# Kernel tuning notes

Measured on AMD Instinct MI355X. Metric: run time of the kernel, lower is better.

Reference implementation:

```python
import jax, jax.numpy as jnp
import numpy as np

# OGB feature vocab sizes
ATOM_DIMS = [119, 4, 12, 12, 10, 6, 6, 2, 2]
BOND_DIMS = [5, 6, 2]
ATOM_OFF = np.concatenate([[0], np.cumsum(ATOM_DIMS)[:-1]]).astype(np.int32)
BOND_OFF = np.concatenate([[0], np.cumsum(BOND_DIMS)[:-1]]).astype(np.int32)
SCHEDULE_LEN = 5   # len(train_schedule) == len(eval_schedule)
NUM_GRAPHS = 12000
BN_EPS = 1e-5

N_NODES, N_EDGES, HIDDEN, NUM_TASKS = 300000, 600000, 128, 128


def setup_inputs() -> dict:
    key = jax.random.key(0)
    ks = jax.random.split(key, 16)
    x = jax.random.randint(ks[0], (N_NODES, 9), 0, 2, dtype=jnp.int32)
    edge_index = jax.random.randint(ks[1], (2, N_EDGES), 0, N_NODES, dtype=jnp.int32)
    edge_attr = jax.random.randint(ks[2], (N_EDGES, 3), 0, 2, dtype=jnp.int32)
    batch = jnp.sort(jax.random.randint(ks[3], (N_NODES,), 0, NUM_GRAPHS, dtype=jnp.int32))
    # learned parameters (embedding tables concatenated with offsets)
    atom_emb = jax.random.normal(ks[4], (sum(ATOM_DIMS), HIDDEN), jnp.float32) * 0.1
    bond_emb = jax.random.normal(ks[5], (sum(BOND_DIMS), HIDDEN), jnp.float32) * 0.1
    conv_W = jax.random.normal(ks[6], (HIDDEN, HIDDEN), jnp.float32) * (1.0 / np.sqrt(HIDDEN))
    conv_b = jnp.zeros((HIDDEN,), jnp.float32)
    root_emb = jax.random.normal(ks[7], (HIDDEN,), jnp.float32) * 0.1
    bn_gamma = jnp.ones((HIDDEN,), jnp.float32)
    bn_beta = jnp.zeros((HIDDEN,), jnp.float32)
    bn_mean = jnp.zeros((HIDDEN,), jnp.float32)   # running stats (eval mode)
    bn_var = jnp.ones((HIDDEN,), jnp.float32)
    lin_W = jax.random.normal(ks[8], (NUM_TASKS, HIDDEN), jnp.float32) * (1.0 / np.sqrt(HIDDEN))
    lin_b = jnp.zeros((NUM_TASKS,), jnp.float32)
    return {"x": x, "edge_index": edge_index, "edge_attr": edge_attr, "batch": batch,
            "atom_emb": atom_emb, "bond_emb": bond_emb, "conv_W": conv_W, "conv_b": conv_b,
            "root_emb": root_emb, "bn_gamma": bn_gamma, "bn_beta": bn_beta,
            "bn_mean": bn_mean, "bn_var": bn_var, "lin_W": lin_W, "lin_b": lin_b}


def reference(x, edge_index, edge_attr, batch, atom_emb, bond_emb, conv_W, conv_b,
              root_emb, bn_gamma, bn_beta, bn_mean, bn_var, lin_W, lin_b):
    N = x.shape[0]
    # AtomEncoder / BondEncoder: sum of per-feature embedding lookups
    h = atom_emb[x + jnp.asarray(ATOM_OFF, x.dtype)].sum(axis=1)            # [N, H]
    e = bond_emb[edge_attr + jnp.asarray(BOND_OFF, edge_attr.dtype)].sum(axis=1)  # [E, H]
    row, col = edge_index[0], edge_index[1]
    deg = jax.ops.segment_sum(jnp.ones_like(row, h.dtype), row, num_segments=N) + 1.0  # [N]
    dis = deg ** -0.5                                                        # deg >= 1, no inf
    norm = dis[row] * dis[col]                                               # [E]
    inv_std = bn_gamma / jnp.sqrt(bn_var + BN_EPS)
    for i in range(SCHEDULE_LEN):
        old = h
        z = h @ conv_W.T + conv_b                                            # [N, H]
        # message: norm * relu(x_j + edge_emb), aggregated at target (col) via scatter-add
        msg = norm[:, None] * jax.nn.relu(z[row] + e)                        # [E, H]
        agg = jax.ops.segment_sum(msg, col, num_segments=N)                  # [N, H]
        z = agg + jax.nn.relu(z + root_emb) / deg[:, None]                   # self-loop term
        z = jax.nn.relu(z)
        z = (z - bn_mean) * inv_std + bn_beta                                # BN (eval, running stats)
        # dropout: identity in eval mode
        # NOTE: faithful to source bug: smooth_fac is the loop index i, not schedule[i]
        h = i * old + (1 - i) * z
    # global mean pool over graphs
    counts = jax.ops.segment_sum(jnp.ones((N,), h.dtype), batch, num_segments=NUM_GRAPHS)
    pooled = jax.ops.segment_sum(h, batch, num_segments=NUM_GRAPHS) / jnp.maximum(counts, 1.0)[:, None]
    return pooled @ lin_W.T + lin_b                                          # [num_graphs, num_tasks]
```

## Files before the change

### kernel.cpp

```cpp
#include <hip/hip_runtime.h>

#define HID 128
#define AROWS 173

typedef __attribute__((ext_vector_type(8))) short short8;
typedef __attribute__((ext_vector_type(8))) unsigned short ushort8v;
typedef __attribute__((ext_vector_type(4))) float floatx4;
typedef __attribute__((ext_vector_type(4))) unsigned short ushort4v;

__device__ __forceinline__ unsigned short f2bf(float f) {
    unsigned u = __builtin_bit_cast(unsigned, f);
    u += 0x7FFF + ((u >> 16) & 1);
    return (unsigned short)(u >> 16);
}
__device__ __forceinline__ float bf2f(unsigned short s) {
    unsigned u = ((unsigned)s) << 16;
    return __builtin_bit_cast(float, u);
}

__global__ void fillrd_kernel(float* __restrict__ dis, int* __restrict__ indeg,
                              int* __restrict__ dhist, int N)
{
    int i = blockIdx.x * 256 + threadIdx.x;
    if (i < N) { dis[i] = 0.f; indeg[i] = 0; }
    if (blockIdx.x == 0 && threadIdx.x < 32) dhist[threadIdx.x] = 0;
}

__global__ void diag_kernel(float* __restrict__ out, long n, float val)
{
    long i = (long)blockIdx.x * blockDim.x + threadIdx.x;
    if (i < n) out[i] = val;
}

__global__ __launch_bounds__(256) void tables_kernel(
    const float* __restrict__ conv_W, unsigned short* __restrict__ Wb,
    const float* __restrict__ lin_W, unsigned short* __restrict__ linWb,
    const float* __restrict__ bond_emb, unsigned short* __restrict__ comb,
    const float* __restrict__ gamma, const float* __restrict__ beta,
    const float* __restrict__ mean, const float* __restrict__ var,
    float* __restrict__ bnsc, float* __restrict__ bnsh,
    const float* __restrict__ atom_emb, unsigned short* __restrict__ aeb)
{
    int blk = blockIdx.x;
    int tid = threadIdx.x;
    if (blk < 64) {
        int i = blk * 256 + tid;
        Wb[i] = f2bf(conv_W[i]);
    } else if (blk < 128) {
        int i = (blk - 64) * 256 + tid;
        linWb[i] = f2bf(lin_W[i]);
    } else if (blk < 158) {
        int i = (blk - 128) * 2 + (tid >> 7);
        int c = tid & 127;
        int a0 = i / 12, a1 = (i % 12) / 2, a2 = i % 2;
        comb[i * HID + c] = f2bf(bond_emb[a0 * HID + c] + bond_emb[(5 + a1) * HID + c]
                               + bond_emb[(11 + a2) * HID + c]);
    } else if (blk == 158) {
        if (tid < HID) {
            float sc = gamma[tid] * rsqrtf(var[tid] + 1e-5f);
            bnsc[tid] = sc;
            bnsh[tid] = beta[tid] - mean[tid] * sc;
        }
    } else {
        int i = (blk - 159) * 256 + tid;
        if (i < AROWS * HID) aeb[i] = f2bf(atom_emb[i]);
    }
}

__global__ void hist_kernel(const int* __restrict__ ei, float* __restrict__ dis,
                            int* __restrict__ indeg, int E)
{
    for (int e = blockIdx.x * blockDim.x + threadIdx.x; e < E; e += gridDim.x * blockDim.x) {
        atomicAdd(&dis[ei[e]], 1.f);
        atomicAdd(&indeg[ei[E + e]], 1);
    }
}

__global__ void fdeg_kernel(float* __restrict__ dis, int N)
{
    int n = blockIdx.x * blockDim.x + threadIdx.x;
    if (n < N) dis[n] = rsqrtf(dis[n] + 1.f);
}

__global__ __launch_bounds__(256) void bsum_kernel(
    const int* __restrict__ indeg, int* __restrict__ partial, int N)
{
    __shared__ int s[256];
    int i = blockIdx.x * 256 + threadIdx.x;
    s[threadIdx.x] = (i < N) ? indeg[i] : 0;
    __syncthreads();
    for (int d = 128; d > 0; d >>= 1) {
        if (threadIdx.x < d) s[threadIdx.x] += s[threadIdx.x + d];
        __syncthreads();
    }
    if (threadIdx.x == 0) partial[blockIdx.x] = s[0];
}

__global__ __launch_bounds__(256) void scan1_kernel(
    const int* __restrict__ partial, int* __restrict__ offs,
    int* __restrict__ ptr, int B, int N)
{
    __shared__ int s[256];
    __shared__ int carry_s;
    int tid = threadIdx.x;
    if (tid == 0) carry_s = 0;
    __syncthreads();
    for (int base = 0; base < B; base += 256) {
        int i = base + tid;
        int v = (i < B) ? partial[i] : 0;
        s[tid] = v;
        __syncthreads();
        for (int d = 1; d < 256; d <<= 1) {
            int t = (tid >= d) ? s[tid - d] : 0;
            __syncthreads();
            s[tid] += t;
            __syncthreads();
        }
        int carry = carry_s;
        if (i < B) offs[i] = carry + s[tid] - v;
        __syncthreads();
        if (tid == 0) carry_s = carry + s[255];
        __syncthreads();
    }
    if (tid == 0) ptr[N] = carry_s;
}

__global__ __launch_bounds__(256) void scan2_kernel(
    const int* __restrict__ indeg, const int* __restrict__ offs,
    int* __restrict__ ptr, int* __restrict__ cursor, int N)
{
    __shared__ int s[256];
    int tid = threadIdx.x;
    int i = blockIdx.x * 256 + tid;
    int v = (i < N) ? indeg[i] : 0;
    s[tid] = v;
    __syncthreads();
    for (int d = 1; d < 256; d <<= 1) {
        int t = (tid >= d) ? s[tid - d] : 0;
        __syncthreads();
        s[tid] += t;
        __syncthreads();
    }
    if (i < N) {
        int ex = offs[blockIdx.x] + s[tid] - v;
        ptr[i] = ex;
        cursor[i] = ex;
    }
}

__global__ __launch_bounds__(256) void dhist_kernel(
    const int* __restrict__ ptr, int* __restrict__ dhist, int N)
{
    __shared__ int lh[32];
    int tid = threadIdx.x;
    if (tid < 32) lh[tid] = 0;
    __syncthreads();
    int n = blockIdx.x * 256 + tid;
    if (n < N) {
        int d = ptr[n + 1] - ptr[n];
        if (d > 31) d = 31;
        atomicAdd(&lh[d], 1);
    }
    __syncthreads();
    if (tid < 32 && lh[tid]) atomicAdd(&dhist[tid], lh[tid]);
}

__global__ void dscan_kernel(const int* __restrict__ dhist, int* __restrict__ dcur)
{
    if (threadIdx.x == 0) {
        int s = 0;
        for (int k = 0; k < 32; ++k) { dcur[k] = s; s += dhist[k]; }
    }
}

__global__ __launch_bounds__(256) void dperm_kernel(
    const int* __restrict__ ptr, int* __restrict__ dcur,
    int* __restrict__ perm, int N)
{
    __shared__ int lh[32];
    __shared__ int gb[32];
    int tid = threadIdx.x;
    if (tid < 32) lh[tid] = 0;
    __syncthreads();
    int n = blockIdx.x * 256 + tid;
    int rank = 0, d = 0;
    if (n < N) {
        d = ptr[n + 1] - ptr[n];
        if (d > 31) d = 31;
        rank = atomicAdd(&lh[d], 1);
    }
    __syncthreads();
    if (tid < 32) gb[tid] = lh[tid] ? atomicAdd(&dcur[tid], lh[tid]) : 0;
    __syncthreads();
    if (n < N) perm[gb[d] + rank] = n;
}

__global__ void fillcsr_kernel(const int* __restrict__ ei, const int* __restrict__ attr,
                               const float* __restrict__ dis, int* __restrict__ cursor,
                               int2* __restrict__ edata, int E)
{
    for (int e = blockIdx.x * blockDim.x + threadIdx.x; e < E; e += gridDim.x * blockDim.x) {
        int r   = ei[e];
        int col = ei[E + e];
        int pos = atomicAdd(&cursor[col], 1);
        int ci  = attr[e * 3] * 12 + attr[e * 3 + 1] * 2 + attr[e * 3 + 2];
        float nrm = dis[r] * dis[col];
        int2 ed;
        ed.x = r;
        ed.y = ci | ((int)f2bf(nrm) << 16);
        edata[pos] = ed;
    }
}

__global__ void gptr_kernel(const int* __restrict__ batch, int* __restrict__ gptr,
                            int N, int G)
{
    int n = blockIdx.x * blockDim.x + threadIdx.x;
    if (n >= N) return;
    int b = batch[n];
    int bp = (n == 0) ? -1 : batch[n - 1];
    for (int g = bp + 1; g <= b; ++g) gptr[g] = n;
    if (n == N - 1)
        for (int g = b + 1; g <= G; ++g) gptr[g] = N;
}

template<bool FIRST>
__global__ __launch_bounds__(256) void agg_kernel(
    const int* __restrict__ perm, const int* __restrict__ ptr,
    const int2* __restrict__ edata, const unsigned short* __restrict__ comb,
    const float* __restrict__ dis, const float* __restrict__ root,
    const float* __restrict__ bnsc, const float* __restrict__ bnsh,
    const unsigned short* __restrict__ zb, unsigned short* __restrict__ hb,
    float fi, int N)
{
    long slot = (long)blockIdx.x * 16 + (threadIdx.x >> 4);
    if (slot >= N) return;
    long n = perm[slot];
    int c = (threadIdx.x & 15) * 8;

    ushort8v zv = *reinterpret_cast<const ushort8v*>(zb + n * HID + c);
    ushort8v hv;
    if constexpr (!FIRST) hv = *reinterpret_cast<const ushort8v*>(hb + n * HID + c);
    float di = dis[n];
    float rd = di * di;
    float acc[8];
#pragma unroll
    for (int j = 0; j < 8; ++j) acc[j] = fmaxf(bf2f(zv[j]) + root[c + j], 0.f) * rd;

    int jb = ptr[n], je = ptr[n + 1];
    int j2 = jb;
    for (; j2 + 1 < je; j2 += 2) {
        int2 e0 = edata[j2];
        int2 e1 = edata[j2 + 1];
        ushort8v z0 = *reinterpret_cast<const ushort8v*>(zb + (long)e0.x * HID + c);
        ushort8v z1 = *reinterpret_cast<const ushort8v*>(zb + (long)e1.x * HID + c);
        ushort8v c0 = *reinterpret_cast<const ushort8v*>(comb + (e0.y & 0xFF) * HID + c);
        ushort8v c1 = *reinterpret_cast<const ushort8v*>(comb + (e1.y & 0xFF) * HID + c);
        float n0 = bf2f((unsigned short)(((unsigned)e0.y) >> 16));
        float n1 = bf2f((unsigned short)(((unsigned)e1.y) >> 16));
#pragma unroll
        for (int j = 0; j < 8; ++j) {
            acc[j] += fmaxf(bf2f(z0[j]) + bf2f(c0[j]), 0.f) * n0;
            acc[j] += fmaxf(bf2f(z1[j]) + bf2f(c1[j]), 0.f) * n1;
        }
    }
    if (j2 < je) {
        int2 e0 = edata[j2];
        ushort8v z0 = *reinterpret_cast<const ushort8v*>(zb + (long)e0.x * HID + c);
        ushort8v c0 = *reinterpret_cast<const ushort8v*>(comb + (e0.y & 0xFF) * HID + c);
        float n0 = bf2f((unsigned short)(((unsigned)e0.y) >> 16));
#pragma unroll
        for (int j = 0; j < 8; ++j)
            acc[j] += fmaxf(bf2f(z0[j]) + bf2f(c0[j]), 0.f) * n0;
    }

    ushort8v o;
#pragma unroll
    for (int j = 0; j < 8; ++j) {
        float t = fmaxf(acc[j], 0.f) * bnsc[c + j] + bnsh[c + j];
        float h;
        if constexpr (FIRST) h = t;
        else h = fi * bf2f(hv[j]) + (1.f - fi) * t;
        o[j] = f2bf(h);
    }
    *reinterpret_cast<ushort8v*>(hb + n * HID + c) = o;
}

__device__ __forceinline__ void gemm_from_lds(
    unsigned short (*hs)[132], const unsigned short* __restrict__ Wb,
    const float* __restrict__ bias, unsigned short* __restrict__ zb,
    long base, int N, int tid)
{
    int wave = tid >> 6;
    int lane = tid & 63;
    int l15 = lane & 15;
    int q = lane >> 4;
    int rowl0 = wave * 32;

    short8 a[2][4];
#pragma unroll
    for (int mt = 0; mt < 2; ++mt) {
        int rl = rowl0 + mt * 16 + l15;
#pragma unroll
        for (int kb = 0; kb < 4; ++kb)
            a[mt][kb] = *reinterpret_cast<const short8*>(&hs[rl][q * 8 + kb * 32]);
    }

    floatx4 acc[2][8];
#pragma unroll
    for (int mt = 0; mt < 2; ++mt)
#pragma unroll
        for (int nt = 0; nt < 8; ++nt) {
            floatx4 zz = {0.f, 0.f, 0.f, 0.f};
            acc[mt][nt] = zz;
        }

#pragma unroll
    for (int nt = 0; nt < 8; ++nt) {
        const unsigned short* bp = Wb + (nt * 16 + l15) * HID + q * 8;
#pragma unroll
        for (int kb = 0; kb < 4; ++kb) {
            short8 b = *reinterpret_cast<const short8*>(bp + kb * 32);
            acc[0][nt] = __builtin_amdgcn_mfma_f32_16x16x32_bf16(a[0][kb], b, acc[0][nt], 0, 0, 0);
            acc[1][nt] = __builtin_amdgcn_mfma_f32_16x16x32_bf16(a[1][kb], b, acc[1][nt], 0, 0, 0);
        }
    }

    float bi[8];
#pragma unroll
    for (int nt = 0; nt < 8; ++nt) bi[nt] = bias[nt * 16 + l15];

    __syncthreads();
#pragma unroll
    for (int mt = 0; mt < 2; ++mt)
#pragma unroll
        for (int r = 0; r < 4; ++r) {
            int lr = rowl0 + mt * 16 + q * 4 + r;
#pragma unroll
            for (int nt = 0; nt < 8; ++nt)
                hs[lr][l15 + 16 * nt] = f2bf(acc[mt][nt][r] + bi[nt]);
        }
    __syncthreads();

    int tr = tid >> 4;
    int tc = (tid & 15) * 8;
#pragma unroll
    for (int i = 0; i < 8; ++i) {
        int row = i * 16 + tr;
        long gr = base + row;
        if (gr < N) {
            ushort8v v = *reinterpret_cast<const ushort8v*>(&hs[row][tc]);
            *reinterpret_cast<ushort8v*>(zb + gr * HID + tc) = v;
        }
    }
}

__global__ __launch_bounds__(256) void egemm_kernel(
    const int* __restrict__ x, const unsigned short* __restrict__ aeb,
    const unsigned short* __restrict__ Wb, const float* __restrict__ bias,
    unsigned short* __restrict__ zb, int N)
{
    __shared__ unsigned short hs[128][132];
    __shared__ int xs[128 * 9];
    int tid = threadIdx.x;
    long base = (long)blockIdx.x * 128;
    const int OFF[9] = {0, 119, 123, 135, 147, 157, 163, 169, 171};

    int nb = (N - base < 128) ? (int)(N - base) : 128;
    int cnt = nb * 9;
    for (int i = tid; i < cnt; i += 256) xs[i] = x[base * 9 + i];
    __syncthreads();

    int sn = tid >> 4;
    int cc = (tid & 15) * 8;
#pragma unroll 1
    for (int s = 0; s < 8; ++s) {
        int lr = s * 16 + sn;
        ushort8v o;
        if (lr < nb) {
            float acc[8];
#pragma unroll
            for (int j = 0; j < 8; ++j) acc[j] = 0.f;
#pragma unroll
            for (int f = 0; f < 9; ++f) {
                int idx = xs[lr * 9 + f] + OFF[f];
                ushort8v v = *reinterpret_cast<const ushort8v*>(aeb + (long)idx * HID + cc);
#pragma unroll
                for (int j = 0; j < 8; ++j) acc[j] += bf2f(v[j]);
            }
#pragma unroll
            for (int j = 0; j < 8; ++j) o[j] = f2bf(acc[j]);
        } else {
            ushort8v z8 = {0, 0, 0, 0, 0, 0, 0, 0};
            o = z8;
        }
        *reinterpret_cast<ushort8v*>(&hs[lr][cc]) = o;
    }
    __syncthreads();

    gemm_from_lds(hs, Wb, bias, zb, base, N, tid);
}

__global__ __launch_bounds__(256) void gemm_kernel(
    const unsigned short* __restrict__ hb, const unsigned short* __restrict__ Wb,
    const float* __restrict__ bias, unsigned short* __restrict__ zb, int N)
{
    __shared__ unsigned short st[128][132];
    int tid = threadIdx.x;
    int wave = tid >> 6;
    int lane = tid & 63;
    int l15 = lane & 15;
    int q = lane >> 4;
    long base = (long)blockIdx.x * 128;
    long row0 = base + wave * 32;

#pragma unroll
    for (int mt = 0; mt < 2; ++mt) {
        long rl = row0 + mt * 16 + l15;
        if (rl > (long)N - 1) rl = (long)N - 1;
        const unsigned short* ap = hb + rl * HID + q * 8;
        int lrow = wave * 32 + mt * 16 + l15;
#pragma unroll
        for (int kb = 0; kb < 4; ++kb)
            *reinterpret_cast<ushort8v*>(&st[lrow][q * 8 + kb * 32]) =
                *reinterpret_cast<const ushort8v*>(ap + kb * 32);
    }
    __syncthreads();
    gemm_from_lds(st, Wb, bias, zb, base, N, tid);
}

__global__ __launch_bounds__(256) void linmm_kernel(
    const unsigned short* __restrict__ pb, const unsigned short* __restrict__ Wb,
    const float* __restrict__ bias, float* __restrict__ out, int G)
{
    int wave = threadIdx.x >> 6;
    int lane = threadIdx.x & 63;
    int l15 = lane & 15;
    int q = lane >> 4;
    long row0 = (long)blockIdx.x * 128 + wave * 32;

    short8 a[2][4];
#pragma unroll
    for (int mt = 0; mt < 2; ++mt) {
        long rl = row0 + mt * 16 + l15;
        if (rl > (long)G - 1) rl = (long)G - 1;
        const unsigned short* ap = pb + rl * HID + q * 8;
#pragma unroll
        for (int kb = 0; kb < 4; ++kb)
            a[mt][kb] = *reinterpret_cast<const short8*>(ap + kb * 32);
    }

    floatx4 acc[2][8];
#pragma unroll
    for (int mt = 0; mt < 2; ++mt)
#pragma unroll
        for (int nt = 0; nt < 8; ++nt) {
            floatx4 zz = {0.f, 0.f, 0.f, 0.f};
            acc[mt][nt] = zz;
        }

#pragma unroll
    for (int nt = 0; nt < 8; ++nt) {
        const unsigned short* bp = Wb + (nt * 16 + l15) * HID + q * 8;
#pragma unroll
        for (int kb = 0; kb < 4; ++kb) {
            short8 b = *reinterpret_cast<const short8*>(bp + kb * 32);
            acc[0][nt] = __builtin_amdgcn_mfma_f32_16x16x32_bf16(a[0][kb], b, acc[0][nt], 0, 0, 0);
            acc[1][nt] = __builtin_amdgcn_mfma_f32_16x16x32_bf16(a[1][kb], b, acc[1][nt], 0, 0, 0);
        }
    }

    float bi[8];
#pragma unroll
    for (int nt = 0; nt < 8; ++nt) bi[nt] = bias[nt * 16 + l15];

#pragma unroll
    for (int mt = 0; mt < 2; ++mt)
#pragma unroll
        for (int r = 0; r < 4; ++r) {
            long rr = row0 + mt * 16 + q * 4 + r;
            if (rr < G) {
                float* op = out + rr * HID + l15;
#pragma unroll
                for (int nt = 0; nt < 8; ++nt)
                    op[nt * 16] = acc[mt][nt][r] + bi[nt];
            }
        }
}

__global__ __launch_bounds__(256) void pool_kernel(
    const unsigned short* __restrict__ hb, const int* __restrict__ gptr,
    unsigned short* __restrict__ pb, int G)
{
    int g = blockIdx.x;
    if (g >= G) return;
    int tid = threadIdx.x;
    int sub = tid >> 5;
    int c = (tid & 31) * 4;
    int lo = gptr[g], hi = gptr[g + 1];
    floatx4 s = {0.f, 0.f, 0.f, 0.f};
    for (int n = lo + sub; n < hi; n += 8) {
        ushort4v hv = *reinterpret_cast<const ushort4v*>(hb + (long)n * HID + c);
#pragma unroll
        for (int j = 0; j < 4; ++j) s[j] += bf2f(hv[j]);
    }
    __shared__ float ps[8][HID];
    *reinterpret_cast<floatx4*>(&ps[sub][c]) = s;
    __syncthreads();
    if (tid < HID) {
        float sum = 0.f;
#pragma unroll
        for (int k = 0; k < 8; ++k) sum += ps[k][tid];
        float cnt = (hi > lo) ? (float)(hi - lo) : 1.f;
        pb[(long)g * HID + tid] = f2bf(sum / cnt);
    }
}

extern "C" void kernel_launch(void* const* d_in, const int* in_sizes, int n_in,
                              void* d_out, int out_size, void* d_ws, size_t ws_size,
                              hipStream_t stream)
{
    const int* x          = (const int*)d_in[0];
    const int* ei         = (const int*)d_in[1];
    const int* attr       = (const int*)d_in[2];
    const int* batch      = (const int*)d_in[3];
    const float* atom_emb = (const float*)d_in[4];
    const float* bond_emb = (const float*)d_in[5];
    const float* conv_W   = (const float*)d_in[6];
    const float* conv_b   = (const float*)d_in[7];
    const float* root     = (const float*)d_in[8];
    const float* gamma    = (const float*)d_in[9];
    const float* beta     = (const float*)d_in[10];
    const float* mean     = (const float*)d_in[11];
    const float* var      = (const float*)d_in[12];
    const float* lin_W    = (const float*)d_in[13];
    const float* lin_b    = (const float*)d_in[14];
    float* out = (float*)d_out;

    const int N = in_sizes[0] / 9;
    const int E = in_sizes[1] / 2;
    const int G = out_size / HID;
    const int B = (N + 255) / 256;

    auto al = [](size_t b) { return (b + 255) & ~(size_t)255; };
    const size_t need =
        al((size_t)N * HID * 2) +
        al((size_t)N * HID * 2) +
        al((size_t)(N + 1) * 4) +
        al((size_t)E * 8) +
        al((size_t)N * 4) +
        al((size_t)2048 * 4) * 2 +
        al((size_t)(G + 1) * 4) +
        al((size_t)(G + 128) * HID * 2) +
        al((size_t)60 * HID * 2) +
        al((size_t)HID * 4) * 2 +
        al((size_t)HID * HID * 2) * 2 +
        al((size_t)AROWS * HID * 2) +
        al((size_t)N * 4) +
        al(32 * 4) * 2;

    if (ws_size < need || B > 2048) {
        float v = (B > 2048) ? 3000.f : (1000.f + (float)(ws_size >> 20));
        long n = (long)out_size;
        diag_kernel<<<(int)((n + 255) / 256), 256, 0, stream>>>(out, n, v);
        return;
    }

    char* wsp = (char*)d_ws;
    size_t used = 0;
    auto alloc = [&](size_t bytes) { char* p = wsp + used; used += al(bytes); return p; };
    unsigned short* hb = (unsigned short*)alloc((size_t)N * HID * 2);
    unsigned short* zb = (unsigned short*)alloc((size_t)N * HID * 2);
    int* ptr      = (int*)alloc((size_t)(N + 1) * 4);
    int2* edata   = (int2*)alloc((size_t)E * 8);
    int* indeg    = (int*)alloc((size_t)N * 4);
    int* cursor   = indeg;
    int* partial  = (int*)alloc((size_t)2048 * 4);
    int* offs     = (int*)alloc((size_t)2048 * 4);
    int* gptr     = (int*)alloc((size_t)(G + 1) * 4);
    unsigned short* pb = (unsigned short*)alloc((size_t)(G + 128) * HID * 2);
    float* dis    = (float*)pb;
    unsigned short* comb = (unsigned short*)alloc((size_t)60 * HID * 2);
    float* bnsc   = (float*)alloc((size_t)HID * 4);
    float* bnsh   = (float*)alloc((size_t)HID * 4);
    unsigned short* Wb    = (unsigned short*)alloc((size_t)HID * HID * 2);
    unsigned short* linWb = (unsigned short*)alloc((size_t)HID * HID * 2);
    unsigned short* aeb   = (unsigned short*)alloc((size_t)AROWS * HID * 2);
    int* perm     = (int*)alloc((size_t)N * 4);
    int* dhist    = (int*)alloc(32 * 4);
    int* dcur     = (int*)alloc(32 * 4);

    fillrd_kernel<<<B, 256, 0, stream>>>(dis, indeg, dhist, N);
    tables_kernel<<<246, 256, 0, stream>>>(conv_W, Wb, lin_W, linWb, bond_emb, comb,
                                           gamma, beta, mean, var, bnsc, bnsh,
                                           atom_emb, aeb);
    hist_kernel<<<1024, 256, 0, stream>>>(ei, dis, indeg, E);
    fdeg_kernel<<<B, 256, 0, stream>>>(dis, N);
    bsum_kernel<<<B, 256, 0, stream>>>(indeg, partial, N);
    scan1_kernel<<<1, 256, 0, stream>>>(partial, offs, ptr, B, N);
    scan2_kernel<<<B, 256, 0, stream>>>(indeg, offs, ptr, cursor, N);
    dhist_kernel<<<B, 256, 0, stream>>>(ptr, dhist, N);
    dscan_kernel<<<1, 64, 0, stream>>>(dhist, dcur);
    dperm_kernel<<<B, 256, 0, stream>>>(ptr, dcur, perm, N);
    fillcsr_kernel<<<1024, 256, 0, stream>>>(ei, attr, dis, cursor, edata, E);
    gptr_kernel<<<B, 256, 0, stream>>>(batch, gptr, N, G);

    const int gemm_blocks = (N + 127) / 128;
    const int agg_blocks  = (N + 15) / 16;
    egemm_kernel<<<gemm_blocks, 256, 0, stream>>>(x, aeb, Wb, conv_b, zb, N);
    agg_kernel<true ><<<agg_blocks, 256, 0, stream>>>(perm, ptr, edata, comb, dis,
            root, bnsc, bnsh, zb, hb, 0.f, N);
    const float fis[3] = {2.f, 3.f, 4.f};
    for (int t = 0; t < 3; ++t) {
        gemm_kernel<<<gemm_blocks, 256, 0, stream>>>(hb, Wb, conv_b, zb, N);
        agg_kernel<false><<<agg_blocks, 256, 0, stream>>>(perm, ptr, edata, comb, dis,
                root, bnsc, bnsh, zb, hb, fis[t], N);
    }

    pool_kernel<<<G, 256, 0, stream>>>(hb, gptr, pb, G);
    linmm_kernel<<<(G + 127) / 128, 256, 0, stream>>>(pb, linWb, lin_b, out, G);
}
```

Before: 726.1 us.

## Fuse aggregation with next-layer GEMM and merge small setup kernels

Each aggregation step now also runs the following layer's linear transform: the block's 64 aggregated rows are staged in LDS, multiplied by W with MFMA, and written to a second z buffer that is ping-ponged between layers. This removes the separate gemm kernels along with their re-read of h from global memory. Several small preprocessing kernels (degree rsqrt, degree histogram, histogram scan, graph pointer) are folded into existing ones to cut launch count. The fused path needs an extra N×H bf16 buffer and only runs when the workspace is large enough; the GEMM stage now writes rows scattered in perm order instead of contiguously.

```diff
diff --git a/kernel.cpp b/kernel.cpp
--- a/kernel.cpp
+++ b/kernel.cpp
@@ -76,29 +76,35 @@
     }
 }
 
-__global__ void fdeg_kernel(float* __restrict__ dis, int N)
-{
-    int n = blockIdx.x * blockDim.x + threadIdx.x;
-    if (n < N) dis[n] = rsqrtf(dis[n] + 1.f);
-}
-
 __global__ __launch_bounds__(256) void bsum_kernel(
-    const int* __restrict__ indeg, int* __restrict__ partial, int N)
+    const int* __restrict__ indeg, int* __restrict__ partial,
+    float* __restrict__ dis, int* __restrict__ dhist, int N)
 {
     __shared__ int s[256];
-    int i = blockIdx.x * 256 + threadIdx.x;
-    s[threadIdx.x] = (i < N) ? indeg[i] : 0;
+    __shared__ int lh[32];
+    int tid = threadIdx.x;
+    if (tid < 32) lh[tid] = 0;
+    int i = blockIdx.x * 256 + tid;
+    int v = (i < N) ? indeg[i] : 0;
+    s[tid] = v;
+    if (i < N) {
+        dis[i] = rsqrtf(dis[i] + 1.f);
+        int d = v > 31 ? 31 : v;
+        atomicAdd(&lh[d], 1);
+    }
     __syncthreads();
     for (int d = 128; d > 0; d >>= 1) {
-        if (threadIdx.x < d) s[threadIdx.x] += s[threadIdx.x + d];
+        if (tid < d) s[tid] += s[tid + d];
         __syncthreads();
     }
-    if (threadIdx.x == 0) partial[blockIdx.x] = s[0];
+    if (tid == 0) partial[blockIdx.x] = s[0];
+    if (tid < 32 && lh[tid]) atomicAdd(&dhist[tid], lh[tid]);
 }
 
 __global__ __launch_bounds__(256) void scan1_kernel(
     const int* __restrict__ partial, int* __restrict__ offs,
-    int* __restrict__ ptr, int B, int N)
+    int* __restrict__ ptr, const int* __restrict__ dhist, int* __restrict__ dcur,
+    int B, int N)
 {
     __shared__ int s[256];
     __shared__ int carry_s;
@@ -122,7 +128,11 @@
         if (tid == 0) carry_s = carry + s[255];
         __syncthreads();
     }
-    if (tid == 0) ptr[N] = carry_s;
+    if (tid == 0) {
+        ptr[N] = carry_s;
+        int sum = 0;
+        for (int k = 0; k < 32; ++k) { dcur[k] = sum; sum += dhist[k]; }
+    }
 }
 
 __global__ __launch_bounds__(256) void scan2_kernel(
@@ -145,31 +155,6 @@
         int ex = offs[blockIdx.x] + s[tid] - v;
         ptr[i] = ex;
         cursor[i] = ex;
-    }
-}
-
-__global__ __launch_bounds__(256) void dhist_kernel(
-    const int* __restrict__ ptr, int* __restrict__ dhist, int N)
-{
-    __shared__ int lh[32];
-    int tid = threadIdx.x;
-    if (tid < 32) lh[tid] = 0;
-    __syncthreads();
-    int n = blockIdx.x * 256 + tid;
-    if (n < N) {
-        int d = ptr[n + 1] - ptr[n];
-        if (d > 31) d = 31;
-        atomicAdd(&lh[d], 1);
-    }
-    __syncthreads();
-    if (tid < 32 && lh[tid]) atomicAdd(&dhist[tid], lh[tid]);
-}
-
-__global__ void dscan_kernel(const int* __restrict__ dhist, int* __restrict__ dcur)
-{
-    if (threadIdx.x == 0) {
-        int s = 0;
-        for (int k = 0; k < 32; ++k) { dcur[k] = s; s += dhist[k]; }
     }
 }
 
@@ -197,7 +182,8 @@
 
 __global__ void fillcsr_kernel(const int* __restrict__ ei, const int* __restrict__ attr,
                                const float* __restrict__ dis, int* __restrict__ cursor,
-                               int2* __restrict__ edata, int E)
+                               int2* __restrict__ edata, const int* __restrict__ batch,
+                               int* __restrict__ gptr, int E, int N, int G)
 {
     for (int e = blockIdx.x * blockDim.x + threadIdx.x; e < E; e += gridDim.x * blockDim.x) {
         int r   = ei[e];
@@ -210,34 +196,23 @@
         ed.y = ci | ((int)f2bf(nrm) << 16);
         edata[pos] = ed;
     }
-}
-
-__global__ void gptr_kernel(const int* __restrict__ batch, int* __restrict__ gptr,
-                            int N, int G)
-{
-    int n = blockIdx.x * blockDim.x + threadIdx.x;
-    if (n >= N) return;
-    int b = batch[n];
-    int bp = (n == 0) ? -1 : batch[n - 1];
-    for (int g = bp + 1; g <= b; ++g) gptr[g] = n;
-    if (n == N - 1)
-        for (int g = b + 1; g <= G; ++g) gptr[g] = N;
+    for (int n = blockIdx.x * blockDim.x + threadIdx.x; n < N; n += gridDim.x * blockDim.x) {
+        int b = batch[n];
+        int bp = (n == 0) ? -1 : batch[n - 1];
+        for (int g = bp + 1; g <= b; ++g) gptr[g] = n;
+        if (n == N - 1)
+            for (int g = b + 1; g <= G; ++g) gptr[g] = N;
+    }
 }
 
 template<bool FIRST>
-__global__ __launch_bounds__(256) void agg_kernel(
-    const int* __restrict__ perm, const int* __restrict__ ptr,
-    const int2* __restrict__ edata, const unsigned short* __restrict__ comb,
-    const float* __restrict__ dis, const float* __restrict__ root,
-    const float* __restrict__ bnsc, const float* __restrict__ bnsh,
-    const unsigned short* __restrict__ zb, unsigned short* __restrict__ hb,
-    float fi, int N)
-{
-    long slot = (long)blockIdx.x * 16 + (threadIdx.x >> 4);
-    if (slot >= N) return;
-    long n = perm[slot];
-    int c = (threadIdx.x & 15) * 8;
-
+__device__ __forceinline__ ushort8v agg_node(
+    long n, int c, const int* __restrict__ ptr, const int2* __restrict__ edata,
+    const unsigned short* __restrict__ comb, const float* __restrict__ dis,
+    const float* __restrict__ root, const float* __restrict__ bnsc,
+    const float* __restrict__ bnsh, const unsigned short* __restrict__ zb,
+    const unsigned short* __restrict__ hb, float fi)
+{
     ushort8v zv = *reinterpret_cast<const ushort8v*>(zb + n * HID + c);
     ushort8v hv;
     if constexpr (!FIRST) hv = *reinterpret_cast<const ushort8v*>(hb + n * HID + c);
@@ -283,7 +258,110 @@
         else h = fi * bf2f(hv[j]) + (1.f - fi) * t;
         o[j] = f2bf(h);
     }
+    return o;
+}
+
+template<bool FIRST>
+__global__ __launch_bounds__(256) void agg_kernel(
+    const int* __restrict__ perm, const int* __restrict__ ptr,
+    const int2* __restrict__ edata, const unsigned short* __restrict__ comb,
+    const float* __restrict__ dis, const float* __restrict__ root,
+    const float* __restrict__ bnsc, const float* __restrict__ bnsh,
+    const unsigned short* __restrict__ zb, unsigned short* __restrict__ hb,
+    float fi, int N)
+{
+    long slot = (long)blockIdx.x * 16 + (threadIdx.x >> 4);
+    if (slot >= N) return;
+    long n = perm[slot];
+    int c = (threadIdx.x & 15) * 8;
+    ushort8v o = agg_node<FIRST>(n, c, ptr, edata, comb, dis, root, bnsc, bnsh,
+                                 zb, hb, fi);
     *reinterpret_cast<ushort8v*>(hb + n * HID + c) = o;
+}
+
+template<bool FIRST>
+__global__ __launch_bounds__(256) void fusedag_kernel(
+    const int* __restrict__ perm, const int* __restrict__ ptr,
+    const int2* __restrict__ edata, const unsigned short* __restrict__ comb,
+    const float* __restrict__ dis, const float* __restrict__ root,
+    const float* __restrict__ bnsc, const float* __restrict__ bnsh,
+    const unsigned short* __restrict__ zin, unsigned short* __restrict__ hb,
+    const unsigned short* __restrict__ Wb, const float* __restrict__ bias,
+    unsigned short* __restrict__ zout, float fi, int N)
+{
+    __shared__ unsigned short hs[64][132];
+    int tid = threadIdx.x;
+    long base = (long)blockIdx.x * 64;
+    int sn = tid >> 4;
+    int cc = (tid & 15) * 8;
+
+#pragma unroll 1
+    for (int s = 0; s < 4; ++s) {
+        int lr = s * 16 + sn;
+        long slot = base + lr;
+        ushort8v o = {0, 0, 0, 0, 0, 0, 0, 0};
+        if (slot < N) {
+            long n = perm[slot];
+            o = agg_node<FIRST>(n, cc, ptr, edata, comb, dis, root, bnsc, bnsh,
+                                zin, hb, fi);
+            *reinterpret_cast<ushort8v*>(hb + n * HID + cc) = o;
+        }
+        *reinterpret_cast<ushort8v*>(&hs[lr][cc]) = o;
+    }
+    __syncthreads();
+
+    int wave = tid >> 6;
+    int lane = tid & 63;
+    int l15 = lane & 15;
+    int q = lane >> 4;
+    int row0 = wave * 16;
+
+    short8 a[4];
+#pragma unroll
+    for (int kb = 0; kb < 4; ++kb)
+        a[kb] = *reinterpret_cast<const short8*>(&hs[row0 + l15][q * 8 + kb * 32]);
+
+    floatx4 acc[8];
+#pragma unroll
+    for (int nt = 0; nt < 8; ++nt) {
+        floatx4 zz = {0.f, 0.f, 0.f, 0.f};
+        acc[nt] = zz;
+    }
+#pragma unroll
+    for (int nt = 0; nt < 8; ++nt) {
+        const unsigned short* bp = Wb + (nt * 16 + l15) * HID + q * 8;
+#pragma unroll
+        for (int kb = 0; kb < 4; ++kb) {
+            short8 b = *reinterpret_cast<const short8*>(bp + kb * 32);
+            acc[nt] = __builtin_amdgcn_mfma_f32_16x16x32_bf16(a[kb], b, acc[nt], 0, 0, 0);
+        }
+    }
+
+    float bi[8];
+#pragma unroll
+    for (int nt = 0; nt < 8; ++nt) bi[nt] = bias[nt * 16 + l15];
+
+#pragma unroll
+    for (int r = 0; r < 4; ++r) {
+        int lr = row0 + q * 4 + r;
+#pragma unroll
+        for (int nt = 0; nt < 8; ++nt)
+            hs[lr][l15 + 16 * nt] = f2bf(acc[nt][r] + bi[nt]);
+    }
+    __syncthreads();
+
+    int tr = tid >> 4;
+    int tc = (tid & 15) * 8;
+#pragma unroll
+    for (int i = 0; i < 4; ++i) {
+        int row = i * 16 + tr;
+        long slot = base + row;
+        if (slot < N) {
+            long n = perm[slot];
+            ushort8v v = *reinterpret_cast<const ushort8v*>(&hs[row][tc]);
+            *reinterpret_cast<ushort8v*>(zout + n * HID + tc) = v;
+        }
+    }
 }
 
 __device__ __forceinline__ void gemm_from_lds(
@@ -543,7 +621,7 @@
     const int B = (N + 255) / 256;
 
     auto al = [](size_t b) { return (b + 255) & ~(size_t)255; };
-    const size_t need =
+    const size_t need_base =
         al((size_t)N * HID * 2) +
         al((size_t)N * HID * 2) +
         al((size_t)(N + 1) * 4) +
@@ -558,13 +636,15 @@
         al((size_t)AROWS * HID * 2) +
         al((size_t)N * 4) +
         al(32 * 4) * 2;
-
-    if (ws_size < need || B > 2048) {
+    const size_t need_fused = need_base + al((size_t)N * HID * 2);
+
+    if (ws_size < need_base || B > 2048) {
         float v = (B > 2048) ? 3000.f : (1000.f + (float)(ws_size >> 20));
         long n = (long)out_size;
         diag_kernel<<<(int)((n + 255) / 256), 256, 0, stream>>>(out, n, v);
         return;
     }
+    const bool fused_ok = (ws_size >= need_fused);
 
     char* wsp = (char*)d_ws;
     size_t used = 0;
@@ -589,32 +669,43 @@
     int* perm     = (int*)alloc((size_t)N * 4);
     int* dhist    = (int*)alloc(32 * 4);
     int* dcur     = (int*)alloc(32 * 4);
+    unsigned short* zb2 = (unsigned short*)alloc((size_t)N * HID * 2);
 
     fillrd_kernel<<<B, 256, 0, stream>>>(dis, indeg, dhist, N);
     tables_kernel<<<246, 256, 0, stream>>>(conv_W, Wb, lin_W, linWb, bond_emb, comb,
                                            gamma, beta, mean, var, bnsc, bnsh,
                                            atom_emb, aeb);
     hist_kernel<<<1024, 256, 0, stream>>>(ei, dis, indeg, E);
-    fdeg_kernel<<<B, 256, 0, stream>>>(dis, N);
-    bsum_kernel<<<B, 256, 0, stream>>>(indeg, partial, N);
-    scan1_kernel<<<1, 256, 0, stream>>>(partial, offs, ptr, B, N);
+    bsum_kernel<<<B, 256, 0, stream>>>(indeg, partial, dis, dhist, N);
+    scan1_kernel<<<1, 256, 0, stream>>>(partial, offs, ptr, dhist, dcur, B, N);
     scan2_kernel<<<B, 256, 0, stream>>>(indeg, offs, ptr, cursor, N);
-    dhist_kernel<<<B, 256, 0, stream>>>(ptr, dhist, N);
-    dscan_kernel<<<1, 64, 0, stream>>>(dhist, dcur);
     dperm_kernel<<<B, 256, 0, stream>>>(ptr, dcur, perm, N);
-    fillcsr_kernel<<<1024, 256, 0, stream>>>(ei, attr, dis, cursor, edata, E);
-    gptr_kernel<<<B, 256, 0, stream>>>(batch, gptr, N, G);
-
-    const int gemm_blocks = (N + 127) / 128;
-    const int agg_blocks  = (N + 15) / 16;
+    fillcsr_kernel<<<1024, 256, 0, stream>>>(ei, attr, dis, cursor, edata,
+                                             batch, gptr, E, N, G);
+
+    const int gemm_blocks  = (N + 127) / 128;
+    const int fused_blocks = (N + 63) / 64;
+    const int agg_blocks   = (N + 15) / 16;
     egemm_kernel<<<gemm_blocks, 256, 0, stream>>>(x, aeb, Wb, conv_b, zb, N);
-    agg_kernel<true ><<<agg_blocks, 256, 0, stream>>>(perm, ptr, edata, comb, dis,
-            root, bnsc, bnsh, zb, hb, 0.f, N);
-    const float fis[3] = {2.f, 3.f, 4.f};
-    for (int t = 0; t < 3; ++t) {
-        gemm_kernel<<<gemm_blocks, 256, 0, stream>>>(hb, Wb, conv_b, zb, N);
-        agg_kernel<false><<<agg_blocks, 256, 0, stream>>>(perm, ptr, edata, comb, dis,
-                root, bnsc, bnsh, zb, hb, fis[t], N);
+
+    if (fused_ok) {
+        fusedag_kernel<true ><<<fused_blocks, 256, 0, stream>>>(perm, ptr, edata,
+                comb, dis, root, bnsc, bnsh, zb,  hb, Wb, conv_b, zb2, 0.f, N);
+        fusedag_kernel<false><<<fused_blocks, 256, 0, stream>>>(perm, ptr, edata,
+                comb, dis, root, bnsc, bnsh, zb2, hb, Wb, conv_b, zb,  2.f, N);
+        fusedag_kernel<false><<<fused_blocks, 256, 0, stream>>>(perm, ptr, edata,
+                comb, dis, root, bnsc, bnsh, zb,  hb, Wb, conv_b, zb2, 3.f, N);
+        agg_kernel<false><<<agg_blocks, 256, 0, stream>>>(perm, ptr, edata, comb,
+                dis, root, bnsc, bnsh, zb2, hb, 4.f, N);
+    } else {
+        agg_kernel<true ><<<agg_blocks, 256, 0, stream>>>(perm, ptr, edata, comb,
+                dis, root, bnsc, bnsh, zb, hb, 0.f, N);
+        const float fis[3] = {2.f, 3.f, 4.f};
+        for (int t = 0; t < 3; ++t) {
+            gemm_kernel<<<gemm_blocks, 256, 0, stream>>>(hb, Wb, conv_b, zb, N);
+            agg_kernel<false><<<agg_blocks, 256, 0, stream>>>(perm, ptr, edata, comb,
+                    dis, root, bnsc, bnsh, zb, hb, fis[t], N);
+        }
     }
 
     pool_kernel<<<G, 256, 0, stream>>>(hb, gptr, pb, G);
```

Result: slower. 797.7 us (+9.9%).

## Precompute atom-embedding times conv weight, drop degree-sorted permutation, fuse setup kernels

Applied to the files above, without the earlier changes.

Folds the first layer's linear transform into the atom embedding table (EW = atom_emb @ W^T), so the encoder becomes a pure per-node gather-sum instead of an embedding sum followed by a GEMM. It also removes the degree-bucketing permutation (dhist/dscan/dperm) so aggregation walks nodes in natural order, and fuses fdeg into bsum and gptr into fillcsr to cut launches. The trade-off is that agg loses degree-sorted load balancing across wavefronts. Summing bf16-rounded pre-multiplied rows also changes rounding slightly.

```diff
diff --git a/kernel.cpp b/kernel.cpp
--- a/kernel.cpp
+++ b/kernel.cpp
@@ -18,12 +18,10 @@
     return __builtin_bit_cast(float, u);
 }
 
-__global__ void fillrd_kernel(float* __restrict__ dis, int* __restrict__ indeg,
-                              int* __restrict__ dhist, int N)
+__global__ void fillrd_kernel(float* __restrict__ dis, int* __restrict__ indeg, int N)
 {
     int i = blockIdx.x * 256 + threadIdx.x;
     if (i < N) { dis[i] = 0.f; indeg[i] = 0; }
-    if (blockIdx.x == 0 && threadIdx.x < 32) dhist[threadIdx.x] = 0;
 }
 
 __global__ void diag_kernel(float* __restrict__ out, long n, float val)
@@ -38,8 +36,7 @@
     const float* __restrict__ bond_emb, unsigned short* __restrict__ comb,
     const float* __restrict__ gamma, const float* __restrict__ beta,
     const float* __restrict__ mean, const float* __restrict__ var,
-    float* __restrict__ bnsc, float* __restrict__ bnsh,
-    const float* __restrict__ atom_emb, unsigned short* __restrict__ aeb)
+    float* __restrict__ bnsc, float* __restrict__ bnsh)
 {
     int blk = blockIdx.x;
     int tid = threadIdx.x;
@@ -55,16 +52,29 @@
         int a0 = i / 12, a1 = (i % 12) / 2, a2 = i % 2;
         comb[i * HID + c] = f2bf(bond_emb[a0 * HID + c] + bond_emb[(5 + a1) * HID + c]
                                + bond_emb[(11 + a2) * HID + c]);
-    } else if (blk == 158) {
-        if (tid < HID) {
-            float sc = gamma[tid] * rsqrtf(var[tid] + 1e-5f);
-            bnsc[tid] = sc;
-            bnsh[tid] = beta[tid] - mean[tid] * sc;
-        }
-    } else {
-        int i = (blk - 159) * 256 + tid;
-        if (i < AROWS * HID) aeb[i] = f2bf(atom_emb[i]);
-    }
+    } else if (tid < HID) {
+        float sc = gamma[tid] * rsqrtf(var[tid] + 1e-5f);
+        bnsc[tid] = sc;
+        bnsh[tid] = beta[tid] - mean[tid] * sc;
+    }
+}
+
+__global__ __launch_bounds__(128) void ewk_kernel(
+    const float* __restrict__ atom_emb, const float* __restrict__ conv_W,
+    unsigned short* __restrict__ EWb)
+{
+    int r = blockIdx.x;
+    int c = threadIdx.x;
+    const float* er = atom_emb + (long)r * HID;
+    const float* wr = conv_W + (long)c * HID;
+    float acc = 0.f;
+#pragma unroll 4
+    for (int k = 0; k < HID; k += 4) {
+        floatx4 e4 = *reinterpret_cast<const floatx4*>(er + k);
+        floatx4 w4 = *reinterpret_cast<const floatx4*>(wr + k);
+        acc += e4[0] * w4[0] + e4[1] * w4[1] + e4[2] * w4[2] + e4[3] * w4[3];
+    }
+    EWb[(long)r * HID + c] = f2bf(acc);
 }
 
 __global__ void hist_kernel(const int* __restrict__ ei, float* __restrict__ dis,
@@ -76,24 +86,22 @@
     }
 }
 
-__global__ void fdeg_kernel(float* __restrict__ dis, int N)
-{
-    int n = blockIdx.x * blockDim.x + threadIdx.x;
-    if (n < N) dis[n] = rsqrtf(dis[n] + 1.f);
-}
-
 __global__ __launch_bounds__(256) void bsum_kernel(
-    const int* __restrict__ indeg, int* __restrict__ partial, int N)
+    const int* __restrict__ indeg, int* __restrict__ partial,
+    float* __restrict__ dis, int N)
 {
     __shared__ int s[256];
-    int i = blockIdx.x * 256 + threadIdx.x;
-    s[threadIdx.x] = (i < N) ? indeg[i] : 0;
+    int tid = threadIdx.x;
+    int i = blockIdx.x * 256 + tid;
+    int v = (i < N) ? indeg[i] : 0;
+    s[tid] = v;
+    if (i < N) dis[i] = rsqrtf(dis[i] + 1.f);
     __syncthreads();
     for (int d = 128; d > 0; d >>= 1) {
-        if (threadIdx.x < d) s[threadIdx.x] += s[threadIdx.x + d];
+        if (tid < d) s[tid] += s[tid + d];
         __syncthreads();
     }
-    if (threadIdx.x == 0) partial[blockIdx.x] = s[0];
+    if (tid == 0) partial[blockIdx.x] = s[0];
 }
 
 __global__ __launch_bounds__(256) void scan1_kernel(
@@ -148,56 +156,10 @@
     }
 }
 
-__global__ __launch_bounds__(256) void dhist_kernel(
-    const int* __restrict__ ptr, int* __restrict__ dhist, int N)
-{
-    __shared__ int lh[32];
-    int tid = threadIdx.x;
-    if (tid < 32) lh[tid] = 0;
-    __syncthreads();
-    int n = blockIdx.x * 256 + tid;
-    if (n < N) {
-        int d = ptr[n + 1] - ptr[n];
-        if (d > 31) d = 31;
-        atomicAdd(&lh[d], 1);
-    }
-    __syncthreads();
-    if (tid < 32 && lh[tid]) atomicAdd(&dhist[tid], lh[tid]);
-}
-
-__global__ void dscan_kernel(const int* __restrict__ dhist, int* __restrict__ dcur)
-{
-    if (threadIdx.x == 0) {
-        int s = 0;
-        for (int k = 0; k < 32; ++k) { dcur[k] = s; s += dhist[k]; }
-    }
-}
-
-__global__ __launch_bounds__(256) void dperm_kernel(
-    const int* __restrict__ ptr, int* __restrict__ dcur,
-    int* __restrict__ perm, int N)
-{
-    __shared__ int lh[32];
-    __shared__ int gb[32];
-    int tid = threadIdx.x;
-    if (tid < 32) lh[tid] = 0;
-    __syncthreads();
-    int n = blockIdx.x * 256 + tid;
-    int rank = 0, d = 0;
-    if (n < N) {
-        d = ptr[n + 1] - ptr[n];
-        if (d > 31) d = 31;
-        rank = atomicAdd(&lh[d], 1);
-    }
-    __syncthreads();
-    if (tid < 32) gb[tid] = lh[tid] ? atomicAdd(&dcur[tid], lh[tid]) : 0;
-    __syncthreads();
-    if (n < N) perm[gb[d] + rank] = n;
-}
-
 __global__ void fillcsr_kernel(const int* __restrict__ ei, const int* __restrict__ attr,
                                const float* __restrict__ dis, int* __restrict__ cursor,
-                               int2* __restrict__ edata, int E)
+                               int2* __restrict__ edata, const int* __restrict__ batch,
+                               int* __restrict__ gptr, int E, int N, int G)
 {
     for (int e = blockIdx.x * blockDim.x + threadIdx.x; e < E; e += gridDim.x * blockDim.x) {
         int r   = ei[e];
@@ -210,32 +172,52 @@
         ed.y = ci | ((int)f2bf(nrm) << 16);
         edata[pos] = ed;
     }
-}
-
-__global__ void gptr_kernel(const int* __restrict__ batch, int* __restrict__ gptr,
-                            int N, int G)
-{
-    int n = blockIdx.x * blockDim.x + threadIdx.x;
+    for (int n = blockIdx.x * blockDim.x + threadIdx.x; n < N; n += gridDim.x * blockDim.x) {
+        int b = batch[n];
+        int bp = (n == 0) ? -1 : batch[n - 1];
+        for (int g = bp + 1; g <= b; ++g) gptr[g] = n;
+        if (n == N - 1)
+            for (int g = b + 1; g <= G; ++g) gptr[g] = N;
+    }
+}
+
+__global__ __launch_bounds__(256) void enc_kernel(
+    const int* __restrict__ x, const unsigned short* __restrict__ EWb,
+    const float* __restrict__ bias, unsigned short* __restrict__ zb, int N)
+{
+    long n = (long)blockIdx.x * 16 + (threadIdx.x >> 4);
     if (n >= N) return;
-    int b = batch[n];
-    int bp = (n == 0) ? -1 : batch[n - 1];
-    for (int g = bp + 1; g <= b; ++g) gptr[g] = n;
-    if (n == N - 1)
-        for (int g = b + 1; g <= G; ++g) gptr[g] = N;
+    int c = (threadIdx.x & 15) * 8;
+    const int OFF[9] = {0, 119, 123, 135, 147, 157, 163, 169, 171};
+
+    float acc[8];
+#pragma unroll
+    for (int j = 0; j < 8; ++j) acc[j] = bias[c + j];
+
+#pragma unroll
+    for (int f = 0; f < 9; ++f) {
+        int idx = x[n * 9 + f] + OFF[f];
+        ushort8v v = *reinterpret_cast<const ushort8v*>(EWb + (long)idx * HID + c);
+#pragma unroll
+        for (int j = 0; j < 8; ++j) acc[j] += bf2f(v[j]);
+    }
+
+    ushort8v o;
+#pragma unroll
+    for (int j = 0; j < 8; ++j) o[j] = f2bf(acc[j]);
+    *reinterpret_cast<ushort8v*>(zb + n * HID + c) = o;
 }
 
 template<bool FIRST>
 __global__ __launch_bounds__(256) void agg_kernel(
-    const int* __restrict__ perm, const int* __restrict__ ptr,
-    const int2* __restrict__ edata, const unsigned short* __restrict__ comb,
-    const float* __restrict__ dis, const float* __restrict__ root,
-    const float* __restrict__ bnsc, const float* __restrict__ bnsh,
-    const unsigned short* __restrict__ zb, unsigned short* __restrict__ hb,
-    float fi, int N)
-{
-    long slot = (long)blockIdx.x * 16 + (threadIdx.x >> 4);
-    if (slot >= N) return;
-    long n = perm[slot];
+    const int* __restrict__ ptr, const int2* __restrict__ edata,
+    const unsigned short* __restrict__ comb, const float* __restrict__ dis,
+    const float* __restrict__ root, const float* __restrict__ bnsc,
+    const float* __restrict__ bnsh, const unsigned short* __restrict__ zb,
+    unsigned short* __restrict__ hb, float fi, int N)
+{
+    long n = (long)blockIdx.x * 16 + (threadIdx.x >> 4);
+    if (n >= N) return;
     int c = (threadIdx.x & 15) * 8;
 
     ushort8v zv = *reinterpret_cast<const ushort8v*>(zb + n * HID + c);
@@ -353,52 +335,6 @@
             *reinterpret_cast<ushort8v*>(zb + gr * HID + tc) = v;
         }
     }
-}
-
-__global__ __launch_bounds__(256) void egemm_kernel(
-    const int* __restrict__ x, const unsigned short* __restrict__ aeb,
-    const unsigned short* __restrict__ Wb, const float* __restrict__ bias,
-    unsigned short* __restrict__ zb, int N)
-{
-    __shared__ unsigned short hs[128][132];
-    __shared__ int xs[128 * 9];
-    int tid = threadIdx.x;
-    long base = (long)blockIdx.x * 128;
-    const int OFF[9] = {0, 119, 123, 135, 147, 157, 163, 169, 171};
-
-    int nb = (N - base < 128) ? (int)(N - base) : 128;
-    int cnt = nb * 9;
-    for (int i = tid; i < cnt; i += 256) xs[i] = x[base * 9 + i];
-    __syncthreads();
-
-    int sn = tid >> 4;
-    int cc = (tid & 15) * 8;
-#pragma unroll 1
-    for (int s = 0; s < 8; ++s) {
-        int lr = s * 16 + sn;
-        ushort8v o;
-        if (lr < nb) {
-            float acc[8];
-#pragma unroll
-            for (int j = 0; j < 8; ++j) acc[j] = 0.f;
-#pragma unroll
-            for (int f = 0; f < 9; ++f) {
-                int idx = xs[lr * 9 + f] + OFF[f];
-                ushort8v v = *reinterpret_cast<const ushort8v*>(aeb + (long)idx * HID + cc);
-#pragma unroll
-                for (int j = 0; j < 8; ++j) acc[j] += bf2f(v[j]);
-            }
-#pragma unroll
-            for (int j = 0; j < 8; ++j) o[j] = f2bf(acc[j]);
-        } else {
-            ushort8v z8 = {0, 0, 0, 0, 0, 0, 0, 0};
-            o = z8;
-        }
-        *reinterpret_cast<ushort8v*>(&hs[lr][cc]) = o;
-    }
-    __syncthreads();
-
-    gemm_from_lds(hs, Wb, bias, zb, base, N, tid);
 }
 
 __global__ __launch_bounds__(256) void gemm_kernel(
@@ -555,9 +491,7 @@
         al((size_t)60 * HID * 2) +
         al((size_t)HID * 4) * 2 +
         al((size_t)HID * HID * 2) * 2 +
-        al((size_t)AROWS * HID * 2) +
-        al((size_t)N * 4) +
-        al(32 * 4) * 2;
+        al((size_t)AROWS * HID * 2);
 
     if (ws_size < need || B > 2048) {
         float v = (B > 2048) ? 3000.f : (1000.f + (float)(ws_size >> 20));
@@ -585,35 +519,28 @@
     float* bnsh   = (float*)alloc((size_t)HID * 4);
     unsigned short* Wb    = (unsigned short*)alloc((size_t)HID * HID * 2);
     unsigned short* linWb = (unsigned short*)alloc((size_t)HID * HID * 2);
-    unsigned short* aeb   = (unsigned short*)alloc((size_t)AROWS * HID * 2);
-    int* perm     = (int*)alloc((size_t)N * 4);
-    int* dhist    = (int*)alloc(32 * 4);
-    int* dcur     = (int*)alloc(32 * 4);
-
-    fillrd_kernel<<<B, 256, 0, stream>>>(dis, indeg, dhist, N);
-    tables_kernel<<<246, 256, 0, stream>>>(conv_W, Wb, lin_W, linWb, bond_emb, comb,
-                                           gamma, beta, mean, var, bnsc, bnsh,
-                                           atom_emb, aeb);
+    unsigned short* EWb   = (unsigned short*)alloc((size_t)AROWS * HID * 2);
+
+    fillrd_kernel<<<B, 256, 0, stream>>>(dis, indeg, N);
+    tables_kernel<<<159, 256, 0, stream>>>(conv_W, Wb, lin_W, linWb, bond_emb, comb,
+                                           gamma, beta, mean, var, bnsc, bnsh);
+    ewk_kernel<<<AROWS, 128, 0, stream>>>(atom_emb, conv_W, EWb);
     hist_kernel<<<1024, 256, 0, stream>>>(ei, dis, indeg, E);
-    fdeg_kernel<<<B, 256, 0, stream>>>(dis, N);
-    bsum_kernel<<<B, 256, 0, stream>>>(indeg, partial, N);
+    bsum_kernel<<<B, 256, 0, stream>>>(indeg, partial, dis, N);
     scan1_kernel<<<1, 256, 0, stream>>>(partial, offs, ptr, B, N);
     scan2_kernel<<<B, 256, 0, stream>>>(indeg, offs, ptr, cursor, N);
-    dhist_kernel<<<B, 256, 0, stream>>>(ptr, dhist, N);
-    dscan_kernel<<<1, 64, 0, stream>>>(dhist, dcur);
-    dperm_kernel<<<B, 256, 0, stream>>>(ptr, dcur, perm, N);
-    fillcsr_kernel<<<1024, 256, 0, stream>>>(ei, attr, dis, cursor, edata, E);
-    gptr_kernel<<<B, 256, 0, stream>>>(batch, gptr, N, G);
+    fillcsr_kernel<<<1024, 256, 0, stream>>>(ei, attr, dis, cursor, edata,
+                                             batch, gptr, E, N, G);
 
     const int gemm_blocks = (N + 127) / 128;
-    const int agg_blocks  = (N + 15) / 16;
-    egemm_kernel<<<gemm_blocks, 256, 0, stream>>>(x, aeb, Wb, conv_b, zb, N);
-    agg_kernel<true ><<<agg_blocks, 256, 0, stream>>>(perm, ptr, edata, comb, dis,
+    const int node_blocks = (N + 15) / 16;
+    enc_kernel<<<node_blocks, 256, 0, stream>>>(x, EWb, conv_b, zb, N);
+    agg_kernel<true ><<<node_blocks, 256, 0, stream>>>(ptr, edata, comb, dis,
             root, bnsc, bnsh, zb, hb, 0.f, N);
     const float fis[3] = {2.f, 3.f, 4.f};
     for (int t = 0; t < 3; ++t) {
         gemm_kernel<<<gemm_blocks, 256, 0, stream>>>(hb, Wb, conv_b, zb, N);
-        agg_kernel<false><<<agg_blocks, 256, 0, stream>>>(perm, ptr, edata, comb, dis,
+        agg_kernel<false><<<node_blocks, 256, 0, stream>>>(ptr, edata, comb, dis,
                 root, bnsc, bnsh, zb, hb, fis[t], N);
     }
 
```

Result: faster. 660.3 us (-9.1%).
